# Performance work log

Measured on AMD Instinct MI355X. Metric: run time of the kernel, lower is better.

## Reference

```python
import jax, jax.numpy as jnp
import numpy as np
import math

B, S, D = 4, 2048, 1024
WINDOW = 10  # window_size; attends to |i-j| <= WINDOW//2


def setup_inputs() -> dict:
    key = jax.random.key(0)
    ks = jax.random.split(key, 9)
    sc = 1.0 / math.sqrt(D)
    return {
        "x": jax.random.normal(ks[0], (B, S, D), dtype=jnp.float32),
        "Wq": jax.random.normal(ks[1], (D, D), dtype=jnp.float32) * sc,
        "bq": jnp.zeros((D,), dtype=jnp.float32),
        "Wk": jax.random.normal(ks[2], (D, D), dtype=jnp.float32) * sc,
        "bk": jnp.zeros((D,), dtype=jnp.float32),
        "Wv": jax.random.normal(ks[3], (D, D), dtype=jnp.float32) * sc,
        "bv": jnp.zeros((D,), dtype=jnp.float32),
        "Wo": jax.random.normal(ks[4], (D, D), dtype=jnp.float32) * sc,
        "bo": jnp.zeros((D,), dtype=jnp.float32),
    }


def _local_mask(seq_len: int, window_size: int) -> jnp.ndarray:
    # row i attends to columns [i - w//2, i + w//2] inclusive -> |i - j| <= w//2
    i = jnp.arange(seq_len)[:, None]
    j = jnp.arange(seq_len)[None, :]
    return jnp.abs(i - j) <= (window_size // 2)  # [S, S] bool


def reference(x, Wq, bq, Wk, bk, Wv, bv, Wo, bo):
    # nn.Linear: y = x @ W.T + b
    Q = x @ Wq.T + bq  # [B, S, D]
    K = x @ Wk.T + bk
    V = x @ Wv.T + bv
    scores = jnp.einsum("bqd,bkd->bqk", Q, K) / jnp.float32(math.sqrt(D))
    mask = _local_mask(x.shape[1], WINDOW)
    scores = jnp.where(mask[None, :, :], scores, jnp.float32(-1e9))
    attn = jax.nn.softmax(scores, axis=-1)  # [B, S, S]
    context = jnp.einsum("bqk,bkd->bqd", attn, V)
    output = context @ Wo.T + bo
    return output, attn
```

## Files before the change

### kernel.cpp

```cpp
#include <hip/hip_runtime.h>
#include <hip/hip_bf16.h>
#include <cstdint>
#include <cstddef>


typedef __attribute__((ext_vector_type(8))) short bf16x8;
typedef __attribute__((ext_vector_type(4))) float f32x4;
typedef __attribute__((ext_vector_type(8))) unsigned short ushortx8;

#define GPTR(x) ((const __attribute__((address_space(1))) void*)(x))
#define LPTR(x) ((__attribute__((address_space(3))) void*)(x))

__device__ __forceinline__ unsigned short f2bf(float f) {
    __hip_bfloat16 h = __float2bfloat16(f);
    unsigned short u;
    __builtin_memcpy(&u, &h, 2);
    return u;
}
__device__ __forceinline__ float bf2f(unsigned short u) {
    unsigned int x = ((unsigned int)u) << 16;
    float f;
    __builtin_memcpy(&f, &x, 4);
    return f;
}

__global__ void cvt_all(const float* __restrict__ x,
                        const float* __restrict__ Wq, const float* __restrict__ Wk,
                        const float* __restrict__ Wv, const float* __restrict__ Wo,
                        unsigned short* __restrict__ xh,
                        unsigned short* __restrict__ Wcat,
                        unsigned short* __restrict__ Woh) {
    const int idx = blockIdx.x * blockDim.x + threadIdx.x;
    const float* src;
    unsigned short* dst;
    int s_off, d_off;
    if (idx < 2097152) {
        src = x; dst = xh; s_off = idx; d_off = idx;
    } else {
        const int r   = idx - 2097152;
        const int seg = r >> 18;
        const int off = r & 262143;
        src   = (seg == 0) ? Wq : (seg == 1) ? Wk : (seg == 2) ? Wv : Wo;
        dst   = (seg < 3) ? Wcat : Woh;
        s_off = off;
        d_off = (seg < 3) ? (seg << 18) + off : off;
    }
    f32x4 v = reinterpret_cast<const f32x4*>(src)[s_off];
    ushort4 o;
    o.x = f2bf(v[0]); o.y = f2bf(v[1]); o.z = f2bf(v[2]); o.w = f2bf(v[3]);
    reinterpret_cast<ushort4*>(dst)[d_off] = o;
}

__device__ __forceinline__ void gemm_core(const unsigned short* __restrict__ A,
                                          const unsigned short* __restrict__ Bw,
                                          int K, int tm, int tn,
                                          unsigned short* As, unsigned short* Bs,
                                          f32x4 (&acc)[4][4]) {
    const int tid  = threadIdx.x;
    const int lane = tid & 63;
    const int w    = tid >> 6;
    const int wr   = w >> 1;
    const int wc   = w & 1;

    const int lrow8 = lane >> 3;
    const int lcolb = (lane & 7) << 4;

    const char* Abase = (const char*)(A + (size_t)tm * 128 * (size_t)K);
    const char* Bbase = (const char*)(Bw + (size_t)tn * 128 * (size_t)K);
    const size_t rstride = (size_t)K * 2;

    const int nk = K >> 6;
    for (int t = 0; t < nk; ++t) {
        const size_t k0b = ((size_t)t << 6) * 2;
#pragma unroll
        for (int ii = 0; ii < 4; ++ii) {
            const int c    = (w << 2) + ii;
            const int row  = (c << 3) + lrow8;
            const int csrc = lcolb ^ ((row & 7) << 4);
            __builtin_amdgcn_global_load_lds(
                GPTR(Abase + (size_t)row * rstride + k0b + (size_t)csrc),
                LPTR((char*)As + (c << 10)), 16, 0, 0);
            __builtin_amdgcn_global_load_lds(
                GPTR(Bbase + (size_t)row * rstride + k0b + (size_t)csrc),
                LPTR((char*)Bs + (c << 10)), 16, 0, 0);
        }
        __syncthreads();

#pragma unroll
        for (int kk = 0; kk < 2; ++kk) {
            bf16x8 af[4], bfr[4];
            const int cb = (kk << 6) + ((lane >> 4) << 4);
#pragma unroll
            for (int m = 0; m < 4; ++m) {
                const int row = (wr << 6) + (m << 4) + (lane & 15);
                af[m] = *reinterpret_cast<const bf16x8*>(
                    (const char*)As + row * 128 + (cb ^ ((row & 7) << 4)));
            }
#pragma unroll
            for (int n = 0; n < 4; ++n) {
                const int row = (wc << 6) + (n << 4) + (lane & 15);
                bfr[n] = *reinterpret_cast<const bf16x8*>(
                    (const char*)Bs + row * 128 + (cb ^ ((row & 7) << 4)));
            }
#pragma unroll
            for (int m = 0; m < 4; ++m)
#pragma unroll
                for (int n = 0; n < 4; ++n)
                    acc[m][n] = __builtin_amdgcn_mfma_f32_16x16x32_bf16(
                        af[m], bfr[n], acc[m][n], 0, 0, 0);
        }
        __syncthreads();
    }
}

__launch_bounds__(256, 2)
__global__ void gemm_qkv(const unsigned short* __restrict__ A,
                         const unsigned short* __restrict__ Bw,
                         const float* __restrict__ bq, const float* __restrict__ bk,
                         const float* __restrict__ bv,
                         unsigned short* __restrict__ C, int M, int N, int K) {
    __shared__ unsigned short As[128 * 64];
    __shared__ unsigned short Bs[128 * 64];
    f32x4 acc[4][4];
#pragma unroll
    for (int m = 0; m < 4; ++m)
#pragma unroll
        for (int n = 0; n < 4; ++n) acc[m][n] = (f32x4){0.f, 0.f, 0.f, 0.f};

    gemm_core(A, Bw, K, blockIdx.x, blockIdx.y, As, Bs, acc);

    const int lane = threadIdx.x & 63;
    const int w    = threadIdx.x >> 6;
    const int wr   = w >> 1, wc = w & 1;
    const int seg  = blockIdx.y >> 3;
    const float* bp = (seg == 0) ? bq : (seg == 1) ? bk : bv;

    const int col0 = (blockIdx.y << 7) + (wc << 6) + (lane & 15);
    const int row0 = (blockIdx.x << 7) + (wr << 6) + ((lane >> 4) << 2);
#pragma unroll
    for (int n = 0; n < 4; ++n) {
        const int col = col0 + (n << 4);
        const float bb = bp[col & 1023];
#pragma unroll
        for (int m = 0; m < 4; ++m) {
            const int row = row0 + (m << 4);
#pragma unroll
            for (int r = 0; r < 4; ++r)
                C[(size_t)(row + r) * (size_t)N + col] = f2bf(acc[m][n][r] + bb);
        }
    }
}

__launch_bounds__(256, 2)
__global__ void gemm_out(const unsigned short* __restrict__ A,
                         const unsigned short* __restrict__ Bw,
                         const float* __restrict__ bias,
                         float* __restrict__ C, int M, int N, int K) {
    __shared__ unsigned short As[128 * 64];
    __shared__ unsigned short Bs[128 * 64];
    f32x4 acc[4][4];
#pragma unroll
    for (int m = 0; m < 4; ++m)
#pragma unroll
        for (int n = 0; n < 4; ++n) acc[m][n] = (f32x4){0.f, 0.f, 0.f, 0.f};

    gemm_core(A, Bw, K, blockIdx.x, blockIdx.y, As, Bs, acc);

    const int lane = threadIdx.x & 63;
    const int w    = threadIdx.x >> 6;
    const int wr   = w >> 1, wc = w & 1;
    const int col0 = (blockIdx.y << 7) + (wc << 6) + (lane & 15);
    const int row0 = (blockIdx.x << 7) + (wr << 6) + ((lane >> 4) << 2);
#pragma unroll
    for (int n = 0; n < 4; ++n) {
        const int col = col0 + (n << 4);
        const float bb = bias[col];
#pragma unroll
        for (int m = 0; m < 4; ++m) {
            const int row = row0 + (m << 4);
#pragma unroll
            for (int r = 0; r < 4; ++r)
                C[(size_t)(row + r) * (size_t)N + col] = acc[m][n][r] + bb;
        }
    }
}

__launch_bounds__(256, 4)
__global__ void attn_band_kernel(const unsigned short* __restrict__ QKV,
                                 float* __restrict__ attn,
                                 unsigned short* __restrict__ ctx) {
    __shared__ float psm[4][16];
    const int bid  = blockIdx.x;
    const int rb   = (bid & 7) * 256 + (bid >> 3);
    const int w    = threadIdx.x >> 6;
    const int lane = threadIdx.x & 63;
    const int g    = (rb << 2) + w;
    const int b    = g >> 11;
    const int i    = g & 2047;

    const unsigned short* qrow = QKV + (size_t)g * 3072;
    float qf[16];
    {
        ushortx8 qa = *reinterpret_cast<const ushortx8*>(qrow + (lane << 4));
        ushortx8 qb = *reinterpret_cast<const ushortx8*>(qrow + (lane << 4) + 8);
#pragma unroll
        for (int t = 0; t < 8; ++t) { qf[t] = bf2f(qa[t]); qf[8 + t] = bf2f(qb[t]); }
    }

    float s[11];
#pragma unroll
    for (int jj = 0; jj < 11; ++jj) {
        const int j = i - 5 + jj;
        const bool valid = ((unsigned)j < 2048u);
        const int jc = min(max(j, 0), 2047);
        const unsigned short* krow = QKV + ((size_t)(b << 11) + jc) * 3072 + 1024;
        ushortx8 ka = *reinterpret_cast<const ushortx8*>(krow + (lane << 4));
        ushortx8 kb = *reinterpret_cast<const ushortx8*>(krow + (lane << 4) + 8);
        float d = 0.f;
#pragma unroll
        for (int t = 0; t < 8; ++t)
            d += qf[t] * bf2f(ka[t]) + qf[8 + t] * bf2f(kb[t]);
#pragma unroll
        for (int off = 32; off >= 1; off >>= 1) d += __shfl_xor(d, off, 64);
        s[jj] = valid ? d * 0.03125f : -1e30f;
    }

    float mx = s[0];
#pragma unroll
    for (int jj = 1; jj < 11; ++jj) mx = fmaxf(mx, s[jj]);
    float p[11], sum = 0.f;
#pragma unroll
    for (int jj = 0; jj < 11; ++jj) { p[jj] = expf(s[jj] - mx); sum += p[jj]; }
    const float inv = 1.0f / sum;

    if (lane == 0) {
#pragma unroll
        for (int jj = 0; jj < 11; ++jj) psm[w][jj] = p[jj] * inv;
    }
    __syncthreads();

    const int lo = i - 5;
    float* arow = attn + (size_t)g * 2048;
#pragma unroll
    for (int e = 0; e < 8; ++e) {
        const int c0 = (e << 8) + (lane << 2);
        f32x4 v = (f32x4){0.f, 0.f, 0.f, 0.f};
        if (c0 + 3 >= lo && c0 <= lo + 10) {
#pragma unroll
            for (int t = 0; t < 4; ++t) {
                const int d = c0 + t - lo;
                if ((unsigned)d < 11u) v[t] = psm[w][d];
            }
        }
        *reinterpret_cast<f32x4*>(arow + c0) = v;
    }

    float cacc[16];
#pragma unroll
    for (int t = 0; t < 16; ++t) cacc[t] = 0.f;
#pragma unroll
    for (int jj = 0; jj < 11; ++jj) {
        const int j  = i - 5 + jj;
        const int jc = min(max(j, 0), 2047);
        const float pj = p[jj] * inv;
        const unsigned short* vrow = QKV + ((size_t)(b << 11) + jc) * 3072 + 2048;
        ushortx8 va = *reinterpret_cast<const ushortx8*>(vrow + (lane << 4));
        ushortx8 vb = *reinterpret_cast<const ushortx8*>(vrow + (lane << 4) + 8);
#pragma unroll
        for (int t = 0; t < 8; ++t) {
            cacc[t]     += pj * bf2f(va[t]);
            cacc[8 + t] += pj * bf2f(vb[t]);
        }
    }
    unsigned short* cp = ctx + (size_t)g * 1024 + (lane << 4);
    ushortx8 oa, ob;
#pragma unroll
    for (int t = 0; t < 8; ++t) { oa[t] = f2bf(cacc[t]); ob[t] = f2bf(cacc[8 + t]); }
    *reinterpret_cast<ushortx8*>(cp)     = oa;
    *reinterpret_cast<ushortx8*>(cp + 8) = ob;
}

extern "C" void kernel_launch(void* const* d_in, const int* in_sizes, int n_in,
                              void* d_out, int out_size, void* d_ws, size_t ws_size,
                              hipStream_t stream) {
    const float* x  = (const float*)d_in[0];
    const float* Wq = (const float*)d_in[1];
    const float* bq = (const float*)d_in[2];
    const float* Wk = (const float*)d_in[3];
    const float* bk = (const float*)d_in[4];
    const float* Wv = (const float*)d_in[5];
    const float* bv = (const float*)d_in[6];
    const float* Wo = (const float*)d_in[7];
    const float* bo = (const float*)d_in[8];

    const size_t MS = 8192, DD = 1024;

    float* out  = (float*)d_out;
    float* attn = out + MS * DD;

    char* ws = (char*)d_ws;
    unsigned short* xh   = (unsigned short*)ws; ws += MS * DD * 2;
    unsigned short* Wcat = (unsigned short*)ws; ws += 3 * DD * DD * 2;
    unsigned short* Woh  = (unsigned short*)ws; ws += DD * DD * 2;
    unsigned short* QKV  = (unsigned short*)ws; ws += MS * 3 * DD * 2;
    unsigned short* ctx  = (unsigned short*)ws; ws += MS * DD * 2;

    cvt_all<<<dim3(12288), dim3(256), 0, stream>>>(x, Wq, Wk, Wv, Wo, xh, Wcat, Woh);

    gemm_qkv<<<dim3(64, 24), dim3(256), 0, stream>>>(xh, Wcat, bq, bk, bv,
                                                     QKV, 8192, 3072, 1024);

    attn_band_kernel<<<dim3(2048), dim3(256), 0, stream>>>(QKV, attn, ctx);

    gemm_out<<<dim3(64, 8), dim3(256), 0, stream>>>(ctx, Woh, bo, out, 8192, 1024, 1024);
}
```

Baseline: 133.1 us.

## Replace QKV GEMM with 256x256 double-buffered 8-wave pipelined kernel

Replaces the 128x128 QKV projection GEMM with a 512-thread kernel computing 256x256 tiles. It double-buffers LDS, streams the next K-slice through direct global-to-LDS loads in four phases interleaved with MFMA work, and raises wave priority around the MFMA blocks. It also remaps block IDs into XCD-grouped chunks to improve L2 locality. The aim is to overlap memory traffic with compute and raise arithmetic intensity. In exchange it uses 128KB of LDS per block and more registers, which limits occupancy, and it issues many more barriers.

After: 149.3 us. 1.12x slower.

```diff
diff --git a/kernel.cpp b/kernel.cpp
--- a/kernel.cpp
+++ b/kernel.cpp
@@ -51,6 +51,138 @@
     reinterpret_cast<ushort4*>(dst)[d_off] = o;
 }
 
+
+__device__ __forceinline__ void stage_half(const char* gtile, size_t rstride,
+                                           size_t k0b, unsigned short* ltile,
+                                           int h1, int w, int lane) {
+    const int r0   = (w << 4) + (lane >> 3);
+    const int colb = (lane & 7) << 4;
+#pragma unroll
+    for (int q = 0; q < 2; ++q) {
+        const int rt   = h1 * 128 + r0 + q * 8;
+        const int csrc = colb ^ ((rt & 7) << 4);
+        __builtin_amdgcn_global_load_lds(
+            GPTR(gtile + (size_t)rt * rstride + k0b + (size_t)csrc),
+            LPTR((char*)ltile + (size_t)(h1 * 16384 + w * 2048 + q * 1024)),
+            16, 0, 0);
+    }
+}
+
+__launch_bounds__(512, 2)
+__global__ void gemm_qkv_8ph(const unsigned short* __restrict__ A,
+                             const unsigned short* __restrict__ Bw,
+                             const float* __restrict__ bq,
+                             const float* __restrict__ bk,
+                             const float* __restrict__ bv,
+                             unsigned short* __restrict__ C,
+                             int M, int N, int K) {
+    __shared__ unsigned short As[2][256 * 64];
+    __shared__ unsigned short Bs[2][256 * 64];
+
+    const int tid  = threadIdx.x;
+    const int lane = tid & 63;
+    const int w    = tid >> 6;
+    const int wr   = w >> 2;
+    const int wc   = w & 3;
+
+    const int nb    = gridDim.x;
+    const int chunk = nb >> 3;
+    const int sid   = (blockIdx.x & 7) * chunk + (blockIdx.x >> 3);
+    const int ntn   = N >> 8;
+    const int tm    = sid / ntn;
+    const int tn    = sid % ntn;
+
+    f32x4 acc[8][4];
+#pragma unroll
+    for (int m = 0; m < 8; ++m)
+#pragma unroll
+        for (int n = 0; n < 4; ++n) acc[m][n] = (f32x4){0.f, 0.f, 0.f, 0.f};
+
+    const size_t rstride = (size_t)K * 2;
+    const char* Ag = (const char*)(A + (size_t)tm * 256 * (size_t)K);
+    const char* Bg = (const char*)(Bw + (size_t)tn * 256 * (size_t)K);
+
+#pragma unroll
+    for (int h = 0; h < 4; ++h)
+        stage_half(h < 2 ? Ag : Bg, rstride, 0,
+                   h < 2 ? As[0] : Bs[0], h & 1, w, lane);
+    asm volatile("s_waitcnt vmcnt(0)" ::: "memory");
+    __builtin_amdgcn_sched_barrier(0);
+    __builtin_amdgcn_s_barrier();
+
+    const int NT = K >> 6;
+    unsigned short* Acur = As[0]; unsigned short* Bcur = Bs[0];
+    unsigned short* Anxt = As[1]; unsigned short* Bnxt = Bs[1];
+
+    const int swz = (lane & 7) << 4;
+    const int cb0 = (lane >> 4) << 4;
+
+    for (int t = 0; t < NT; ++t) {
+        const bool   sv  = (t + 1 < NT);
+        const size_t k0b = (size_t)(t + 1) << 7;
+        bf16x8 a[4], b[4];
+#pragma unroll
+        for (int kk = 0; kk < 2; ++kk) {
+#pragma unroll
+            for (int mh = 0; mh < 2; ++mh) {
+                if (mh == 0) {
+#pragma unroll
+                    for (int n = 0; n < 4; ++n) {
+                        const int row = wc * 64 + n * 16 + (lane & 15);
+                        b[n] = *reinterpret_cast<const bf16x8*>(
+                            (const char*)Bcur + row * 128 + ((kk * 64 + cb0) ^ swz));
+                    }
+                }
+#pragma unroll
+                for (int m = 0; m < 4; ++m) {
+                    const int row = wr * 128 + mh * 64 + m * 16 + (lane & 15);
+                    a[m] = *reinterpret_cast<const bf16x8*>(
+                        (const char*)Acur + row * 128 + ((kk * 64 + cb0) ^ swz));
+                }
+                if (sv) {
+                    const int h = kk * 2 + mh;
+                    stage_half(h < 2 ? Ag : Bg, rstride, k0b,
+                               h < 2 ? Anxt : Bnxt, h & 1, w, lane);
+                }
+                __builtin_amdgcn_sched_barrier(0);
+                __builtin_amdgcn_s_barrier();
+                asm volatile("s_waitcnt lgkmcnt(0)" ::: "memory");
+                __builtin_amdgcn_sched_barrier(0);
+                __builtin_amdgcn_s_setprio(1);
+#pragma unroll
+                for (int m = 0; m < 4; ++m)
+#pragma unroll
+                    for (int n = 0; n < 4; ++n)
+                        acc[mh * 4 + m][n] = __builtin_amdgcn_mfma_f32_16x16x32_bf16(
+                            a[m], b[n], acc[mh * 4 + m][n], 0, 0, 0);
+                __builtin_amdgcn_s_setprio(0);
+                __builtin_amdgcn_s_barrier();
+            }
+        }
+        asm volatile("s_waitcnt vmcnt(0)" ::: "memory");
+        __builtin_amdgcn_sched_barrier(0);
+        __builtin_amdgcn_s_barrier();
+        unsigned short* ta = Acur; Acur = Anxt; Anxt = ta;
+        unsigned short* tb = Bcur; Bcur = Bnxt; Bnxt = tb;
+    }
+
+    const int col0 = tn * 256 + wc * 64 + (lane & 15);
+    const int row0 = tm * 256 + wr * 128 + ((lane >> 4) << 2);
+#pragma unroll
+    for (int n = 0; n < 4; ++n) {
+        const int col = col0 + n * 16;
+        const int seg = col >> 10;
+        const float bb = (seg == 0 ? bq : seg == 1 ? bk : bv)[col & 1023];
+#pragma unroll
+        for (int m = 0; m < 8; ++m) {
+            const int row = row0 + m * 16;
+#pragma unroll
+            for (int r = 0; r < 4; ++r)
+                C[(size_t)(row + r) * (size_t)N + col] = f2bf(acc[m][n][r] + bb);
+        }
+    }
+}
+
 __device__ __forceinline__ void gemm_core(const unsigned short* __restrict__ A,
                                           const unsigned short* __restrict__ Bw,
                                           int K, int tm, int tn,
@@ -110,44 +242,6 @@
                         af[m], bfr[n], acc[m][n], 0, 0, 0);
         }
         __syncthreads();
-    }
-}
-
-__launch_bounds__(256, 2)
-__global__ void gemm_qkv(const unsigned short* __restrict__ A,
-                         const unsigned short* __restrict__ Bw,
-                         const float* __restrict__ bq, const float* __restrict__ bk,
-                         const float* __restrict__ bv,
-                         unsigned short* __restrict__ C, int M, int N, int K) {
-    __shared__ unsigned short As[128 * 64];
-    __shared__ unsigned short Bs[128 * 64];
-    f32x4 acc[4][4];
-#pragma unroll
-    for (int m = 0; m < 4; ++m)
-#pragma unroll
-        for (int n = 0; n < 4; ++n) acc[m][n] = (f32x4){0.f, 0.f, 0.f, 0.f};
-
-    gemm_core(A, Bw, K, blockIdx.x, blockIdx.y, As, Bs, acc);
-
-    const int lane = threadIdx.x & 63;
-    const int w    = threadIdx.x >> 6;
-    const int wr   = w >> 1, wc = w & 1;
-    const int seg  = blockIdx.y >> 3;
-    const float* bp = (seg == 0) ? bq : (seg == 1) ? bk : bv;
-
-    const int col0 = (blockIdx.y << 7) + (wc << 6) + (lane & 15);
-    const int row0 = (blockIdx.x << 7) + (wr << 6) + ((lane >> 4) << 2);
-#pragma unroll
-    for (int n = 0; n < 4; ++n) {
-        const int col = col0 + (n << 4);
-        const float bb = bp[col & 1023];
-#pragma unroll
-        for (int m = 0; m < 4; ++m) {
-            const int row = row0 + (m << 4);
-#pragma unroll
-            for (int r = 0; r < 4; ++r)
-                C[(size_t)(row + r) * (size_t)N + col] = f2bf(acc[m][n][r] + bb);
-        }
     }
 }
 
@@ -307,8 +401,8 @@
 
     cvt_all<<<dim3(12288), dim3(256), 0, stream>>>(x, Wq, Wk, Wv, Wo, xh, Wcat, Woh);
 
-    gemm_qkv<<<dim3(64, 24), dim3(256), 0, stream>>>(xh, Wcat, bq, bk, bv,
-                                                     QKV, 8192, 3072, 1024);
+    gemm_qkv_8ph<<<dim3(384), dim3(512), 0, stream>>>(xh, Wcat, bq, bk, bv,
+                                                      QKV, 8192, 3072, 1024);
 
     attn_band_kernel<<<dim3(2048), dim3(256), 0, stream>>>(QKV, attn, ctx);
 
```
